# Performance work log

Measured on AMD Instinct MI355X. Metric: run time of the kernel, lower is better.

## Reference

```python
import jax, jax.numpy as jnp
import numpy as np

B = 4096          # graph pairs in batch
NPG = 40          # nodes per molecular graph
N = B * NPG       # total nodes per drug batch
EPG = 160         # directed edges per graph
E = B * EPG
F_IN = 78         # atom feature dim
HID = 128
HEADS = 4
ADD = 8           # additional features (concentrations)
BN_EPS = 1e-5
D0 = HEADS * HID          # 512
CMB = 4 * HID + ADD       # 2 drugs * (mean||max of 128) + ADD = 520


def setup_inputs() -> dict:
    key = jax.random.key(0)
    ks = iter(jax.random.split(key, 64))
    def nrm(shape, s=0.1):
        return jax.random.normal(next(ks), shape, jnp.float32) * s
    def pos(shape):  # positive running variances
        return jax.random.uniform(next(ks), shape, jnp.float32, 0.5, 1.5)
    offs = jnp.repeat(jnp.arange(B, dtype=jnp.int32) * NPG, EPG)
    def edges():
        return jax.random.randint(next(ks), (2, E), 0, NPG, dtype=jnp.int32) + offs[None, :]
    batch = jnp.repeat(jnp.arange(B, dtype=jnp.int32), NPG)
    inp = dict(
        x_a=nrm((N, F_IN), 1.0), edge_a=edges(), batch_a=batch,
        x_b=nrm((N, F_IN), 1.0), edge_b=edges(), batch_b=batch,
        addf=nrm((B, ADD), 1.0),
        # shared GAT encoder params
        gW0=nrm((F_IN, D0)), gb0=nrm((D0,)), gas0=nrm((D0,)), gad0=nrm((D0,)),
        gW1=nrm((D0, D0)), gb1=nrm((D0,)), gas1=nrm((D0,)), gad1=nrm((D0,)),
        gW2=nrm((D0, HID)), gb2=nrm((HID,)), gas2=nrm((HID,)), gad2=nrm((HID,)),
        bn0g=pos((D0,)), bn0b=nrm((D0,)), bn0m=nrm((D0,)), bn0v=pos((D0,)),
        bn1g=pos((D0,)), bn1b=nrm((D0,)), bn1m=nrm((D0,)), bn1v=pos((D0,)),
        bn2g=pos((HID,)), bn2b=nrm((HID,)), bn2m=nrm((HID,)), bn2v=pos((HID,)),
        # combination MLP params (Linear + eval BatchNorm stats)
        mW0=nrm((CMB, 2 * HID)), mb0=nrm((2 * HID,)),
        mg0=pos((2 * HID,)), mbe0=nrm((2 * HID,)), mm0=nrm((2 * HID,)), mv0=pos((2 * HID,)),
        mW1=nrm((2 * HID, HID)), mb1=nrm((HID,)),
        mg1=pos((HID,)), mbe1=nrm((HID,)), mm1=nrm((HID,)), mv1=pos((HID,)),
        mW2=nrm((HID, 1)), mb2=nrm((1,)),
    )
    return inp


def _bn(x, g, b, m, v):
    return (x - m) * jax.lax.rsqrt(v + BN_EPS) * g + b


def _gat(x, src, dst, W, b, a_src, a_dst, heads, ch, concat):
    """PyG GATConv (eval): linear, per-head additive attention with
    leaky_relu(0.2), segment-softmax over incoming edges (self-loops included)."""
    n = x.shape[0]
    h = (x @ W).reshape(n, heads, ch)                     # [N, H, C]
    es = jnp.sum(h * a_src.reshape(1, heads, ch), -1)     # [N, H]
    ed = jnp.sum(h * a_dst.reshape(1, heads, ch), -1)     # [N, H]
    e = jax.nn.leaky_relu(es[src] + ed[dst], 0.2)         # [E', H]
    emax = jax.ops.segment_max(e, dst, num_segments=n)
    ex = jnp.exp(e - emax[dst])
    den = jax.ops.segment_sum(ex, dst, num_segments=n)
    alpha = ex / den[dst]                                 # [E', H]
    out = jax.ops.segment_sum(h[src] * alpha[..., None], dst, num_segments=n)
    out = out.reshape(n, heads * ch) if concat else jnp.mean(out, axis=1)
    return out + b


def _encode(x, edge, batch, p):
    n = x.shape[0]
    sl = jnp.arange(n, dtype=edge.dtype)                  # self-loops (PyG default)
    src = jnp.concatenate([edge[0], sl])
    dst = jnp.concatenate([edge[1], sl])
    x = _gat(x, src, dst, p['gW0'], p['gb0'], p['gas0'], p['gad0'], HEADS, HID, True)
    x = jax.nn.relu(_bn(x, p['bn0g'], p['bn0b'], p['bn0m'], p['bn0v']))
    x = _gat(x, src, dst, p['gW1'], p['gb1'], p['gas1'], p['gad1'], HEADS, HID, True)
    x = jax.nn.relu(_bn(x, p['bn1g'], p['bn1b'], p['bn1m'], p['bn1v']))
    x = _gat(x, src, dst, p['gW2'], p['gb2'], p['gas2'], p['gad2'], 1, HID, False)
    x = _bn(x, p['bn2g'], p['bn2b'], p['bn2m'], p['bn2v'])  # no relu on last layer
    cnt = jax.ops.segment_sum(jnp.ones((n, 1), x.dtype), batch, num_segments=B)
    x_mean = jax.ops.segment_sum(x, batch, num_segments=B) / cnt
    x_max = jax.ops.segment_max(x, batch, num_segments=B)
    return jnp.concatenate([x_mean, x_max], axis=1)        # [B, 2*HID]


def reference(x_a, edge_a, batch_a, x_b, edge_b, batch_b, addf,
              gW0, gb0, gas0, gad0, gW1, gb1, gas1, gad1, gW2, gb2, gas2, gad2,
              bn0g, bn0b, bn0m, bn0v, bn1g, bn1b, bn1m, bn1v, bn2g, bn2b, bn2m, bn2v,
              mW0, mb0, mg0, mbe0, mm0, mv0, mW1, mb1, mg1, mbe1, mm1, mv1, mW2, mb2):
    p = dict(gW0=gW0, gb0=gb0, gas0=gas0, gad0=gad0, gW1=gW1, gb1=gb1, gas1=gas1,
             gad1=gad1, gW2=gW2, gb2=gb2, gas2=gas2, gad2=gad2,
             bn0g=bn0g, bn0b=bn0b, bn0m=bn0m, bn0v=bn0v,
             bn1g=bn1g, bn1b=bn1b, bn1m=bn1m, bn1v=bn1v,
             bn2g=bn2g, bn2b=bn2b, bn2m=bn2m, bn2v=bn2v)
    emb_a = _encode(x_a, edge_a, batch_a, p)
    emb_b = _encode(x_b, edge_b, batch_b, p)
    c = jnp.concatenate([emb_a, emb_b, addf], axis=1)      # [B, 520]
    h = jax.nn.relu(_bn(c @ mW0 + mb0, mg0, mbe0, mm0, mv0))
    h = jax.nn.relu(_bn(h @ mW1 + mb1, mg1, mbe1, mm1, mv1))
    out = jax.nn.sigmoid(h @ mW2 + mb2)
    return jnp.squeeze(out, -1)                            # [B]
```

## Files before the change

### kernel.cpp

```cpp
#include <hip/hip_runtime.h>
#include <stdint.h>

#define B_GRAPHS 4096
#define NPG 40
#define NTOT (B_GRAPHS * NPG)
#define EPG 160
#define ETOT (B_GRAPHS * EPG)
#define ESL 200
#define F_IN 78
#define KP0 96
#define HID 128
#define D0 512
#define CMB 520
#define BN_EPS 1e-5f
#define AST 48

typedef short bf16x8 __attribute__((ext_vector_type(8)));
typedef float floatx4 __attribute__((ext_vector_type(4)));

__device__ inline float b2f(unsigned short u) {
    union { float f; uint32_t i; } v; v.i = ((uint32_t)u) << 16; return v.f;
}
__device__ inline unsigned short f2b(float f) {
    union { float f; uint32_t i; } v; v.f = f;
    uint32_t x = v.i;
    return (unsigned short)((x + 0x7fffu + ((x >> 16) & 1u)) >> 16);
}
__device__ inline float lo16(uint32_t u) {
    union { float f; uint32_t i; } v; v.i = u << 16; return v.f;
}
__device__ inline float hi16(uint32_t u) {
    union { float f; uint32_t i; } v; v.i = u & 0xffff0000u; return v.f;
}
__device__ inline unsigned int fenc(float f) {
    unsigned int b = __float_as_uint(f);
    return (b & 0x80000000u) ? ~b : (b | 0x80000000u);
}
__device__ inline float fdec(unsigned int u) {
    unsigned int b = (u & 0x80000000u) ? (u & 0x7fffffffu) : ~u;
    return __uint_as_float(b);
}
__device__ inline int htoff(int ch, int s) {
    int chunk = s >> 3, within = s & 7;
    return ch * 40 + (((chunk + ch) % 5) << 3) + within;
}
__device__ inline void gl2lds16(const unsigned short* g, unsigned short* l) {
    __builtin_amdgcn_global_load_lds(
        (const __attribute__((address_space(1))) unsigned int*)g,
        (__attribute__((address_space(3))) unsigned int*)l, 16, 0, 0);
}

__global__ __launch_bounds__(256)
void write_code_kernel(float* __restrict__ out, int n, float S)
{
    int i = blockIdx.x * 256 + threadIdx.x;
    if (i < n) out[i] = (i == 0) ? S : 0.f;
}

__global__ __launch_bounds__(256)
void convw_kernel(const float* __restrict__ W, unsigned short* __restrict__ Wt,
                  int K, int N, int Kp)
{
    int t = blockIdx.x * 256 + threadIdx.x;
    if (t >= N * Kp) return;
    int n = t / Kp, k = t - n * Kp;
    Wt[t] = (k < K) ? f2b(W[(size_t)k * N + n]) : 0;
}

__global__ __launch_bounds__(256)
void convx_kernel(const float* __restrict__ X, unsigned short* __restrict__ Xb, int M)
{
    int t = blockIdx.x * 256 + threadIdx.x;
    if (t >= M * KP0) return;
    int r = t / KP0, k = t - r * KP0;
    Xb[t] = (k < F_IN) ? f2b(X[(size_t)r * F_IN + k]) : 0;
}

__global__ __launch_bounds__(256)
void gemm_mfma_kernel(const unsigned short* __restrict__ A,
                      const unsigned short* __restrict__ Bt,
                      unsigned short* __restrict__ C,
                      int M, int K, int N)
{
    __shared__ __align__(16) unsigned short As[128 * 32];
    __shared__ __align__(16) unsigned short Bs[128 * 32];
    const int tid  = threadIdx.x;
    const int lane = tid & 63, w = tid >> 6;
    const int quad = lane >> 4, l16 = lane & 15;
    const int wm = w >> 1, wn = w & 1;
    const int row0 = blockIdx.y * 128, col0 = blockIdx.x * 128;

    floatx4 acc[4][4];
    #pragma unroll
    for (int mi = 0; mi < 4; mi++)
        #pragma unroll
        for (int ni = 0; ni < 4; ni++)
            acc[mi][ni] = (floatx4){0.f, 0.f, 0.f, 0.f};

    int srow[2], scg[2];
    #pragma unroll
    for (int it = 0; it < 2; it++) {
        int L = it * 4096 + w * 1024 + lane * 16;
        int r = L >> 6;
        int cp = (L >> 4) & 3;
        srow[it] = r;
        scg[it]  = cp ^ ((r >> 1) & 3);
    }

    for (int k0 = 0; k0 < K; k0 += 32) {
        #pragma unroll
        for (int it = 0; it < 2; it++) {
            int ra = row0 + srow[it]; if (ra >= M) ra = M - 1;
            gl2lds16(A + (size_t)ra * K + k0 + scg[it] * 8,
                     As + (it * 4096 + w * 1024) / 2);
            int rb = col0 + srow[it];
            gl2lds16(Bt + (size_t)rb * K + k0 + scg[it] * 8,
                     Bs + (it * 4096 + w * 1024) / 2);
        }
        __syncthreads();

        bf16x8 fA[4], fB[4];
        #pragma unroll
        for (int mi = 0; mi < 4; mi++) {
            int r = wm * 64 + mi * 16 + l16;
            __builtin_memcpy(&fA[mi], &As[r * 32 + ((quad ^ ((r >> 1) & 3)) * 8)], 16);
        }
        #pragma unroll
        for (int ni = 0; ni < 4; ni++) {
            int r = wn * 64 + ni * 16 + l16;
            __builtin_memcpy(&fB[ni], &Bs[r * 32 + ((quad ^ ((r >> 1) & 3)) * 8)], 16);
        }
        #pragma unroll
        for (int mi = 0; mi < 4; mi++)
            #pragma unroll
            for (int ni = 0; ni < 4; ni++)
                acc[mi][ni] = __builtin_amdgcn_mfma_f32_16x16x32_bf16(
                    fB[ni], fA[mi], acc[mi][ni], 0, 0, 0);
        __syncthreads();
    }

    #pragma unroll
    for (int mi = 0; mi < 4; mi++) {
        int row = row0 + wm * 64 + mi * 16 + l16;
        if (row < M) {
            #pragma unroll
            for (int ni = 0; ni < 4; ni++) {
                floatx4 a = acc[mi][ni];
                unsigned int p0 = (unsigned int)f2b(a[0]) | ((unsigned int)f2b(a[1]) << 16);
                unsigned int p1 = (unsigned int)f2b(a[2]) | ((unsigned int)f2b(a[3]) << 16);
                *(uint2*)(C + (size_t)row * N + col0 + wn * 64 + ni * 16 + quad * 4) =
                    make_uint2(p0, p1);
            }
        }
    }
}

__global__ __launch_bounds__(256)
void gat4_fused_kernel(unsigned short* __restrict__ H,
                       const int* __restrict__ edge,
                       const float* __restrict__ avs, const float* __restrict__ avd,
                       const float* __restrict__ bias,
                       const float* __restrict__ bng, const float* __restrict__ bnb,
                       const float* __restrict__ bnm, const float* __restrict__ bnv,
                       int g0)
{
    __shared__ __align__(16) unsigned short ht[D0 * NPG];
    __shared__ float es[4 * NPG], ed[4 * NPG];
    __shared__ unsigned int Mu[4 * NPG];
    __shared__ float den[4 * NPG];
    __shared__ __align__(16) unsigned char cnt[NPG * 48];
    __shared__ short2 eloc[ESL];
    const int tid = threadIdx.x;
    const int lane = tid & 63, w = tid >> 6;
    const int quad = lane >> 4, l16 = lane & 15;
    const int gg = g0 + blockIdx.x;
    unsigned short* Hg = H + (size_t)blockIdx.x * NPG * D0;

    for (int i = tid; i < NPG * 48 / 4; i += 256) ((unsigned int*)cnt)[i] = 0u;
    if (tid < 4 * NPG) { Mu[tid] = 0u; den[tid] = 0.f; }
    for (int i = tid; i < ESL; i += 256) {
        if (i < EPG) {
            int s  = edge[(size_t)gg * EPG + i] - gg * NPG;
            int dd = edge[(size_t)ETOT + (size_t)gg * EPG + i] - gg * NPG;
            eloc[i] = make_short2((short)s, (short)dd);
        } else {
            short v = (short)(i - EPG);
            eloc[i] = make_short2(v, v);
        }
    }
    for (int u = tid; u < 64 * (NPG / 4); u += 256) {
        int c8 = u & 63, gi = u >> 6;
        const unsigned short* src = Hg + (size_t)(4 * gi) * D0 + c8 * 8;
        uint4 v0 = *(const uint4*)(src);
        uint4 v1 = *(const uint4*)(src + D0);
        uint4 v2 = *(const uint4*)(src + 2 * D0);
        uint4 v3 = *(const uint4*)(src + 3 * D0);
        unsigned int a0[4] = {v0.x, v0.y, v0.z, v0.w};
        unsigned int a1[4] = {v1.x, v1.y, v1.z, v1.w};
        unsigned int a2[4] = {v2.x, v2.y, v2.z, v2.w};
        unsigned int a3[4] = {v3.x, v3.y, v3.z, v3.w};
        #pragma unroll
        for (int k = 0; k < 8; k++) {
            const int ws = k >> 1, sh = (k & 1) * 16;
            unsigned int w0 = ((a0[ws] >> sh) & 0xffffu) | (((a1[ws] >> sh) & 0xffffu) << 16);
            unsigned int w1 = ((a2[ws] >> sh) & 0xffffu) | (((a3[ws] >> sh) & 0xffffu) << 16);
            *(uint2*)&ht[htoff(c8 * 8 + k, 4 * gi)] = make_uint2(w0, w1);
        }
    }
    __syncthreads();

    {
        float as0=0,as1=0,as2=0,as3=0, ad0=0,ad1=0,ad2=0,ad3=0;
        for (int ci = 0; ci < 32; ci++) {
            int c = quad + ci * 4;
            int chv = w * 128 + c;
            uint2 hv = *(const uint2*)&ht[htoff(chv, 4 * l16)];
            float h0 = lo16(hv.x), h1 = hi16(hv.x), h2 = lo16(hv.y), h3 = hi16(hv.y);
            float vs = avs[chv], vd = avd[chv];
            as0 += h0*vs; as1 += h1*vs; as2 += h2*vs; as3 += h3*vs;
            ad0 += h0*vd; ad1 += h1*vd; ad2 += h2*vd; ad3 += h3*vd;
        }
        #define RED4(x) x += __shfl_xor(x, 16); x += __shfl_xor(x, 32);
        RED4(as0) RED4(as1) RED4(as2) RED4(as3)
        RED4(ad0) RED4(ad1) RED4(ad2) RED4(ad3)
        #undef RED4
        if (quad == 0) {
            float rs[4] = {as0, as1, as2, as3};
            float rd[4] = {ad0, ad1, ad2, ad3};
            #pragma unroll
            for (int rr = 0; rr < 4; rr++) {
                int node = 4 * l16 + rr;
                if (node < NPG) { es[w * NPG + node] = rs[rr]; ed[w * NPG + node] = rd[rr]; }
            }
        }
    }
    for (int e = tid; e < ESL; e += 256) {
        short2 sd = eloc[e];
        atomicAdd((unsigned int*)cnt + ((sd.y * 48 + sd.x) >> 2),
                  1u << ((sd.x & 3) * 8));
    }
    __syncthreads();

    for (int u = tid; u < 4 * ESL; u += 256) {
        int e = u >> 2, hd = u & 3;
        short2 sd = eloc[e];
        float v = es[hd * NPG + sd.x] + ed[hd * NPG + sd.y];
        v = v > 0.f ? v : 0.2f * v;
        atomicMax(&Mu[hd * NPG + sd.y], fenc(v));
    }
    __syncthreads();
    for (int u = tid; u < 4 * ESL; u += 256) {
        int e = u >> 2, hd = u & 3;
        short2 sd = eloc[e];
        float v = es[hd * NPG + sd.x] + ed[hd * NPG + sd.y];
        v = v > 0.f ? v : 0.2f * v;
        float ex = __expf(v - fdec(Mu[hd * NPG + sd.y]));
        atomicAdd(&den[hd * NPG + sd.y], ex);
    }
    __syncthreads();

    {
        bf16x8 ahi[3][2], alo[3][2];
        float esv0[8], esv1[8];
        #pragma unroll
        for (int j = 0; j < 8; j++) {
            esv0[j] = es[w * NPG + quad * 8 + j];
            esv1[j] = (quad == 0) ? es[w * NPG + 32 + j] : 0.f;
        }
        #pragma unroll
        for (int mt = 0; mt < 3; mt++) {
            int dn = mt * 16 + l16;
            bool ok = dn < NPG;
            float edv = 0.f, m = 0.f, di = 0.f;
            uint2 c0 = make_uint2(0u, 0u), c1 = make_uint2(0u, 0u);
            if (ok) {
                edv = ed[w * NPG + dn];
                m = fdec(Mu[w * NPG + dn]);
                di = 1.f / den[w * NPG + dn];
                c0 = *(const uint2*)&cnt[dn * 48 + quad * 8];
                if (quad == 0) c1 = *(const uint2*)&cnt[dn * 48 + 32];
            }
            #pragma unroll
            for (int j = 0; j < 8; j++) {
                unsigned int cb0 = ((j < 4 ? c0.x : c0.y) >> ((j & 3) * 8)) & 0xffu;
                float v0 = esv0[j] + edv;
                v0 = v0 > 0.f ? v0 : 0.2f * v0;
                float a0 = (ok && cb0) ? (float)cb0 * __expf(v0 - m) * di : 0.f;
                unsigned short hb0 = f2b(a0);
                ahi[mt][0][j] = (short)hb0;
                alo[mt][0][j] = (short)f2b(a0 - b2f(hb0));

                unsigned int cb1 = ((j < 4 ? c1.x : c1.y) >> ((j & 3) * 8)) & 0xffu;
                float v1 = esv1[j] + edv;
                v1 = v1 > 0.f ? v1 : 0.2f * v1;
                float a1 = (ok && quad == 0 && cb1) ? (float)cb1 * __expf(v1 - m) * di : 0.f;
                unsigned short hb1 = f2b(a1);
                ahi[mt][1][j] = (short)hb1;
                alo[mt][1][j] = (short)f2b(a1 - b2f(hb1));
            }
        }
        const floatx4 z = {0.f, 0.f, 0.f, 0.f};
        for (int nt = 0; nt < 8; nt++) {
            const int ch0 = w * 128 + nt * 16;
            bf16x8 b0, b1 = {0,0,0,0,0,0,0,0};
            __builtin_memcpy(&b0, &ht[htoff(ch0 + l16, quad * 8)], 16);
            if (quad == 0) __builtin_memcpy(&b1, &ht[htoff(ch0 + l16, 32)], 16);
            floatx4 acc0 = z, acc1 = z, acc2 = z;
            acc0 = __builtin_amdgcn_mfma_f32_16x16x32_bf16(ahi[0][0], b0, acc0, 0, 0, 0);
            acc1 = __builtin_amdgcn_mfma_f32_16x16x32_bf16(ahi[1][0], b0, acc1, 0, 0, 0);
            acc2 = __builtin_amdgcn_mfma_f32_16x16x32_bf16(ahi[2][0], b0, acc2, 0, 0, 0);
            acc0 = __builtin_amdgcn_mfma_f32_16x16x32_bf16(alo[0][0], b0, acc0, 0, 0, 0);
            acc1 = __builtin_amdgcn_mfma_f32_16x16x32_bf16(alo[1][0], b0, acc1, 0, 0, 0);
            acc2 = __builtin_amdgcn_mfma_f32_16x16x32_bf16(alo[2][0], b0, acc2, 0, 0, 0);
            acc0 = __builtin_amdgcn_mfma_f32_16x16x32_bf16(ahi[0][1], b1, acc0, 0, 0, 0);
            acc1 = __builtin_amdgcn_mfma_f32_16x16x32_bf16(ahi[1][1], b1, acc1, 0, 0, 0);
            acc2 = __builtin_amdgcn_mfma_f32_16x16x32_bf16(ahi[2][1], b1, acc2, 0, 0, 0);
            acc0 = __builtin_amdgcn_mfma_f32_16x16x32_bf16(alo[0][1], b1, acc0, 0, 0, 0);
            acc1 = __builtin_amdgcn_mfma_f32_16x16x32_bf16(alo[1][1], b1, acc1, 0, 0, 0);
            acc2 = __builtin_amdgcn_mfma_f32_16x16x32_bf16(alo[2][1], b1, acc2, 0, 0, 0);
            const int c = ch0 + l16;
            float scl = rsqrtf(bnv[c] + BN_EPS) * bng[c];
            float sft = (bias[c] - bnm[c]) * scl + bnb[c];
            unsigned short* reg = &ht[ch0 * 40];
            #pragma unroll
            for (int mt = 0; mt < 3; mt++) {
                floatx4 a = (mt == 0) ? acc0 : (mt == 1) ? acc1 : acc2;
                #pragma unroll
                for (int rr = 0; rr < 4; rr++) {
                    int dn = mt * 16 + quad * 4 + rr;
                    if (dn < NPG) {
                        float o = a[rr] * scl + sft;
                        o = fmaxf(o, 0.f);
                        reg[dn * 16 + l16] = f2b(o);
                    }
                }
            }
        }
    }
    __syncthreads();
    for (int u = tid; u < NPG * 64; u += 256) {
        int s = u >> 6, c8 = u & 63;
        const unsigned short* reg = &ht[(c8 >> 1) * 16 * 40];
        uint4 v = *(const uint4*)&reg[s * 16 + (c8 & 1) * 8];
        *(uint4*)(Hg + (size_t)s * D0 + c8 * 8) = v;
    }
}

__global__ __launch_bounds__(256)
void gat1_pool_fused_kernel(const unsigned short* __restrict__ H,
                            const int* __restrict__ edge,
                            const float* __restrict__ avs, const float* __restrict__ avd,
                            const float* __restrict__ bias,
                            const float* __restrict__ bng, const float* __restrict__ bnb,
                            const float* __restrict__ bnm, const float* __restrict__ bnv,
                            float* __restrict__ cmb, int colbase, int g0)
{
    __shared__ __align__(16) unsigned short ht[HID * NPG];
    __shared__ float A1f[NPG * AST];
    __shared__ float es[NPG], ed[NPG];
    __shared__ unsigned int Mu[NPG];
    __shared__ float den[NPG];
    __shared__ short2 eloc[ESL];
    const int tid = threadIdx.x;
    const int lane = tid & 63, w = tid >> 6;
    const int quad = lane >> 4, l16 = lane & 15;
    const int gg = g0 + blockIdx.x;
    const unsigned short* Hg = H + (size_t)blockIdx.x * NPG * HID;

    for (int i = tid; i < NPG * AST; i += 256) A1f[i] = 0.f;
    if (tid < NPG) { Mu[tid] = 0u; den[tid] = 0.f; }
    for (int i = tid; i < ESL; i += 256) {
        if (i < EPG) {
            int s  = edge[(size_t)gg * EPG + i] - gg * NPG;
            int dd = edge[(size_t)ETOT + (size_t)gg * EPG + i] - gg * NPG;
            eloc[i] = make_short2((short)s, (short)dd);
        } else {
            short v = (short)(i - EPG);
            eloc[i] = make_short2(v, v);
        }
    }
    for (int u = tid; u < 16 * (NPG / 4); u += 256) {
        int c8 = u & 15, gi = u >> 4;
        const unsigned short* src = Hg + (size_t)(4 * gi) * HID + c8 * 8;
        uint4 v0 = *(const uint4*)(src);
        uint4 v1 = *(const uint4*)(src + HID);
        uint4 v2 = *(const uint4*)(src + 2 * HID);
        uint4 v3 = *(const uint4*)(src + 3 * HID);
        unsigned int a0[4] = {v0.x, v0.y, v0.z, v0.w};
        unsigned int a1[4] = {v1.x, v1.y, v1.z, v1.w};
        unsigned int a2[4] = {v2.x, v2.y, v2.z, v2.w};
        unsigned int a3[4] = {v3.x, v3.y, v3.z, v3.w};
        #pragma unroll
        for (int k = 0; k < 8; k++) {
            const int ws = k >> 1, sh = (k & 1) * 16;
            unsigned int w0 = ((a0[ws] >> sh) & 0xffffu) | (((a1[ws] >> sh) & 0xffffu) << 16);
            unsigned int w1 = ((a2[ws] >> sh) & 0xffffu) | (((a3[ws] >> sh) & 0xffffu) << 16);
            *(uint2*)&ht[htoff(c8 * 8 + k, 4 * gi)] = make_uint2(w0, w1);
        }
    }
    __syncthreads();

    if (w < 2) {
        const float* av = w ? avd : avs;
        float a0=0,a1=0,a2=0,a3=0;
        for (int ci = 0; ci < 32; ci++) {
            int c = quad + ci * 4;
            uint2 hv = *(const uint2*)&ht[htoff(c, 4 * l16)];
            float vc = av[c];
            a0 += lo16(hv.x)*vc; a1 += hi16(hv.x)*vc;
            a2 += lo16(hv.y)*vc; a3 += hi16(hv.y)*vc;
        }
        #define RED4(x) x += __shfl_xor(x, 16); x += __shfl_xor(x, 32);
        RED4(a0) RED4(a1) RED4(a2) RED4(a3)
        #undef RED4
        if (quad == 0) {
            float rv[4] = {a0, a1, a2, a3};
            float* dst = w ? ed : es;
            #pragma unroll
            for (int rr = 0; rr < 4; rr++) {
                int node = 4 * l16 + rr;
                if (node < NPG) dst[node] = rv[rr];
            }
        }
    }
    __syncthreads();
    for (int u = tid; u < ESL; u += 256) {
        short2 sd = eloc[u];
        float v = es[sd.x] + ed[sd.y];
        v = v > 0.f ? v : 0.2f * v;
        atomicMax(&Mu[sd.y], fenc(v));
    }
    __syncthreads();
    for (int u = tid; u < ESL; u += 256) {
        short2 sd = eloc[u];
        float v = es[sd.x] + ed[sd.y];
        v = v > 0.f ? v : 0.2f * v;
        float ex = __expf(v - fdec(Mu[sd.y]));
        atomicAdd(&den[sd.y], ex);
        atomicAdd(&A1f[sd.x * AST + sd.y], ex);
    }
    __syncthreads();
    for (int idx = tid; idx < NPG * AST; idx += 256) {
        int dn = idx % AST;
        float val = A1f[idx];
        unsigned int pw = 0u;
        if (dn < NPG) {
            float a = val / den[dn];
            unsigned short hi = f2b(a);
            float rem = a - b2f(hi);
            pw = (unsigned int)hi | ((unsigned int)f2b(rem) << 16);
        }
        ((unsigned int*)A1f)[idx] = pw;
    }
    __syncthreads();

    {
        const unsigned int* Ap = (const unsigned int*)A1f;
        bf16x8 ahi[3][2], alo[3][2];
        #pragma unroll
        for (int mt = 0; mt < 3; mt++) {
            #pragma unroll
            for (int j = 0; j < 8; j++) {
                unsigned int w0 = Ap[(quad * 8 + j) * AST + mt * 16 + l16];
                ahi[mt][0][j] = (short)(w0 & 0xffffu);
                alo[mt][0][j] = (short)(w0 >> 16);
                unsigned int w1 = (quad == 0) ? Ap[(32 + j) * AST + mt * 16 + l16] : 0u;
                ahi[mt][1][j] = (short)(w1 & 0xffffu);
                alo[mt][1][j] = (short)(w1 >> 16);
            }
        }
        const floatx4 z = {0.f, 0.f, 0.f, 0.f};
        for (int t2 = 0; t2 < 2; t2++) {
            const int ch0 = (w * 2 + t2) * 16;
            bf16x8 b0, b1 = {0,0,0,0,0,0,0,0};
            __builtin_memcpy(&b0, &ht[htoff(ch0 + l16, quad * 8)], 16);
            if (quad == 0) __builtin_memcpy(&b1, &ht[htoff(ch0 + l16, 32)], 16);
            floatx4 acc0 = z, acc1 = z, acc2 = z;
            acc0 = __builtin_amdgcn_mfma_f32_16x16x32_bf16(ahi[0][0], b0, acc0, 0, 0, 0);
            acc1 = __builtin_amdgcn_mfma_f32_16x16x32_bf16(ahi[1][0], b0, acc1, 0, 0, 0);
            acc2 = __builtin_amdgcn_mfma_f32_16x16x32_bf16(ahi[2][0], b0, acc2, 0, 0, 0);
            acc0 = __builtin_amdgcn_mfma_f32_16x16x32_bf16(alo[0][0], b0, acc0, 0, 0, 0);
            acc1 = __builtin_amdgcn_mfma_f32_16x16x32_bf16(alo[1][0], b0, acc1, 0, 0, 0);
            acc2 = __builtin_amdgcn_mfma_f32_16x16x32_bf16(alo[2][0], b0, acc2, 0, 0, 0);
            acc0 = __builtin_amdgcn_mfma_f32_16x16x32_bf16(ahi[0][1], b1, acc0, 0, 0, 0);
            acc1 = __builtin_amdgcn_mfma_f32_16x16x32_bf16(ahi[1][1], b1, acc1, 0, 0, 0);
            acc2 = __builtin_amdgcn_mfma_f32_16x16x32_bf16(ahi[2][1], b1, acc2, 0, 0, 0);
            acc0 = __builtin_amdgcn_mfma_f32_16x16x32_bf16(alo[0][1], b1, acc0, 0, 0, 0);
            acc1 = __builtin_amdgcn_mfma_f32_16x16x32_bf16(alo[1][1], b1, acc1, 0, 0, 0);
            acc2 = __builtin_amdgcn_mfma_f32_16x16x32_bf16(alo[2][1], b1, acc2, 0, 0, 0);
            const int c = ch0 + l16;
            float scl = rsqrtf(bnv[c] + BN_EPS) * bng[c];
            float sft = (bias[c] - bnm[c]) * scl + bnb[c];
            float psum = 0.f, pmax = -1e30f;
            #pragma unroll
            for (int mt = 0; mt < 3; mt++) {
                floatx4 a = (mt == 0) ? acc0 : (mt == 1) ? acc1 : acc2;
                #pragma unroll
                for (int rr = 0; rr < 4; rr++) {
                    int dn = mt * 16 + quad * 4 + rr;
                    if (dn < NPG) {
                        float o = a[rr] * scl + sft;
                        psum += o;
                        pmax = fmaxf(pmax, o);
                    }
                }
            }
            psum += __shfl_xor(psum, 16); psum += __shfl_xor(psum, 32);
            pmax = fmaxf(pmax, __shfl_xor(pmax, 16));
            pmax = fmaxf(pmax, __shfl_xor(pmax, 32));
            if (quad == 0) {
                cmb[(size_t)gg * 512 + colbase + c] = psum * (1.f / NPG);
                cmb[(size_t)gg * 512 + colbase + HID + c] = pmax;
            }
        }
    }
}

__global__ __launch_bounds__(256)
void mlp_kernel(const float* __restrict__ cmb, const float* __restrict__ addf,
                const float* __restrict__ W0, const float* __restrict__ b0,
                const float* __restrict__ g0v, const float* __restrict__ be0,
                const float* __restrict__ m0, const float* __restrict__ v0,
                const float* __restrict__ W1, const float* __restrict__ b1,
                const float* __restrict__ g1v, const float* __restrict__ be1,
                const float* __restrict__ m1, const float* __restrict__ v1,
                const float* __restrict__ W2, const float* __restrict__ b2,
                float* __restrict__ out)
{
    __shared__ float c[CMB];
    __shared__ float h1[256];
    __shared__ float h2[128];
    const int g = blockIdx.x, tid = threadIdx.x;
    for (int i = tid; i < 512; i += 256) c[i] = cmb[(size_t)g * 512 + i];
    if (tid < 8) c[512 + tid] = addf[g * 8 + tid];
    __syncthreads();
    {
        int j = tid;
        float acc = b0[j];
        for (int k = 0; k < CMB; k++) acc += c[k] * W0[k * 256 + j];
        acc = (acc - m0[j]) * rsqrtf(v0[j] + BN_EPS) * g0v[j] + be0[j];
        h1[j] = fmaxf(acc, 0.f);
    }
    __syncthreads();
    if (tid < 128) {
        int j = tid;
        float acc = b1[j];
        for (int k = 0; k < 256; k++) acc += h1[k] * W1[k * 128 + j];
        acc = (acc - m1[j]) * rsqrtf(v1[j] + BN_EPS) * g1v[j] + be1[j];
        h2[j] = fmaxf(acc, 0.f);
    }
    __syncthreads();
    if (tid == 0) {
        float acc = b2[0];
        for (int k = 0; k < 128; k++) acc += h2[k] * W2[k];
        out[g] = 1.f / (1.f + __expf(-acc));
    }
}

extern "C" void kernel_launch(void* const* d_in, const int* in_sizes, int n_in,
                              void* d_out, int out_size, void* d_ws, size_t ws_size,
                              hipStream_t stream)
{
    float* out = (float*)d_out;
    int out_n = out_size < 4096 ? out_size : 4096;

    const float* x_a  = (const float*)d_in[0];
    const int*   edge_a = (const int*)d_in[1];
    const float* x_b  = (const float*)d_in[3];
    const int*   edge_b = (const int*)d_in[4];
    const float* addf = (const float*)d_in[6];
    const float* gW0 = (const float*)d_in[7],  *gb0 = (const float*)d_in[8];
    const float* gas0 = (const float*)d_in[9], *gad0 = (const float*)d_in[10];
    const float* gW1 = (const float*)d_in[11], *gb1 = (const float*)d_in[12];
    const float* gas1 = (const float*)d_in[13], *gad1 = (const float*)d_in[14];
    const float* gW2 = (const float*)d_in[15], *gb2 = (const float*)d_in[16];
    const float* gas2 = (const float*)d_in[17], *gad2 = (const float*)d_in[18];
    const float* bn0g = (const float*)d_in[19], *bn0b = (const float*)d_in[20];
    const float* bn0m = (const float*)d_in[21], *bn0v = (const float*)d_in[22];
    const float* bn1g = (const float*)d_in[23], *bn1b = (const float*)d_in[24];
    const float* bn1m = (const float*)d_in[25], *bn1v = (const float*)d_in[26];
    const float* bn2g = (const float*)d_in[27], *bn2b = (const float*)d_in[28];
    const float* bn2m = (const float*)d_in[29], *bn2v = (const float*)d_in[30];
    const float* mW0 = (const float*)d_in[31], *mb0 = (const float*)d_in[32];
    const float* mg0 = (const float*)d_in[33], *mbe0 = (const float*)d_in[34];
    const float* mm0 = (const float*)d_in[35], *mv0 = (const float*)d_in[36];
    const float* mW1 = (const float*)d_in[37], *mb1 = (const float*)d_in[38];
    const float* mg1 = (const float*)d_in[39], *mbe1 = (const float*)d_in[40];
    const float* mm1 = (const float*)d_in[41], *mv1 = (const float*)d_in[42];
    const float* mW2 = (const float*)d_in[43], *mb2 = (const float*)d_in[44];

    char* p = (char*)d_ws;
    const size_t CMB_BYTES = (size_t)B_GRAPHS * 512 * sizeof(float);
    float* cmb = (float*)p; p += CMB_BYTES;
    unsigned short* W0t = (unsigned short*)p; p += (size_t)D0 * KP0 * 2;
    unsigned short* W1t = (unsigned short*)p; p += (size_t)D0 * D0 * 2;
    unsigned short* W2t = (unsigned short*)p; p += (size_t)HID * D0 * 2;
    size_t used = (size_t)(p - (char*)d_ws);
    const size_t PG = 7680ull + 40960ull + 40960ull;
    int chunk = B_GRAPHS;
    while (chunk > 4 && used + (size_t)chunk * PG > ws_size) chunk >>= 1;
    if (used + (size_t)chunk * PG > ws_size) {
        write_code_kernel<<<(out_n + 255) / 256, 256, 0, stream>>>(out, out_n, 500000.f);
        return;
    }
    unsigned short* Xb = (unsigned short*)p; p += (size_t)chunk * 7680;
    unsigned short* B1 = (unsigned short*)p; p += (size_t)chunk * 40960;
    unsigned short* B2 = (unsigned short*)p;

    convw_kernel<<<(D0 * KP0 + 255) / 256, 256, 0, stream>>>(gW0, W0t, F_IN, D0, KP0);
    convw_kernel<<<(D0 * D0 + 255) / 256, 256, 0, stream>>>(gW1, W1t, D0, D0, D0);
    convw_kernel<<<(HID * D0 + 255) / 256, 256, 0, stream>>>(gW2, W2t, D0, HID, D0);

    for (int drug = 0; drug < 2; drug++) {
        const float* x = drug ? x_b : x_a;
        const int* edge = drug ? edge_b : edge_a;
        int colbase = drug ? 256 : 0;

        for (int g0 = 0; g0 < B_GRAPHS; g0 += chunk) {
            int n = chunk * NPG;
            int gy = (n + 127) / 128;
            convx_kernel<<<(n * KP0 + 255) / 256, 256, 0, stream>>>(
                x + (size_t)g0 * NPG * F_IN, Xb, n);
            gemm_mfma_kernel<<<dim3(D0 / 128, gy), 256, 0, stream>>>(
                Xb, W0t, B1, n, KP0, D0);
            gat4_fused_kernel<<<chunk, 256, 0, stream>>>(
                B1, edge, gas0, gad0, gb0, bn0g, bn0b, bn0m, bn0v, g0);
            gemm_mfma_kernel<<<dim3(D0 / 128, gy), 256, 0, stream>>>(
                B1, W1t, B2, n, D0, D0);
            gat4_fused_kernel<<<chunk, 256, 0, stream>>>(
                B2, edge, gas1, gad1, gb1, bn1g, bn1b, bn1m, bn1v, g0);
            gemm_mfma_kernel<<<dim3(HID / 128, gy), 256, 0, stream>>>(
                B2, W2t, B1, n, D0, HID);
            gat1_pool_fused_kernel<<<chunk, 256, 0, stream>>>(
                B1, edge, gas2, gad2, gb2, bn2g, bn2b, bn2m, bn2v,
                cmb, colbase, g0);
        }
    }
    mlp_kernel<<<B_GRAPHS, 256, 0, stream>>>(
        cmb, addf, mW0, mb0, mg0, mbe0, mm0, mv0,
        mW1, mb1, mg1, mbe1, mm1, mv1, mW2, mb2, out);
}
```

Baseline: 1.489 ms.

## Run combination MLP on MFMA with split bf16 hi/lo and vectorize convx

```diff
diff --git a/kernel.cpp b/kernel.cpp
--- a/kernel.cpp
+++ b/kernel.cpp
@@ -14,6 +14,10 @@
 #define CMB 520
 #define BN_EPS 1e-5f
 #define AST 48
+#define KPM 544
+#define A0ST 552
+#define H1ST 264
+#define H2ST 132
 
 typedef short bf16x8 __attribute__((ext_vector_type(8)));
 typedef float floatx4 __attribute__((ext_vector_type(4)));
@@ -68,12 +72,35 @@
 }
 
 __global__ __launch_bounds__(256)
+void convw_hilo_kernel(const float* __restrict__ W,
+                       unsigned short* __restrict__ Whi,
+                       unsigned short* __restrict__ Wlo,
+                       int K, int N, int Kp)
+{
+    int t = blockIdx.x * 256 + threadIdx.x;
+    if (t >= N * Kp) return;
+    int n = t / Kp, k = t - n * Kp;
+    float x = (k < K) ? W[(size_t)k * N + n] : 0.f;
+    unsigned short hb = f2b(x);
+    Whi[t] = hb;
+    Wlo[t] = f2b(x - b2f(hb));
+}
+
+__global__ __launch_bounds__(256)
 void convx_kernel(const float* __restrict__ X, unsigned short* __restrict__ Xb, int M)
 {
     int t = blockIdx.x * 256 + threadIdx.x;
-    if (t >= M * KP0) return;
-    int r = t / KP0, k = t - r * KP0;
-    Xb[t] = (k < F_IN) ? f2b(X[(size_t)r * F_IN + k]) : 0;
+    if (t >= M * (KP0 / 8)) return;
+    int r = t / (KP0 / 8), c8 = t - r * (KP0 / 8);
+    unsigned int pk[4];
+    #pragma unroll
+    for (int j = 0; j < 4; j++) {
+        int k0 = c8 * 8 + 2 * j, k1 = k0 + 1;
+        float x0 = (k0 < F_IN) ? X[(size_t)r * F_IN + k0] : 0.f;
+        float x1 = (k1 < F_IN) ? X[(size_t)r * F_IN + k1] : 0.f;
+        pk[j] = (unsigned int)f2b(x0) | ((unsigned int)f2b(x1) << 16);
+    }
+    *(uint4*)&Xb[(size_t)r * KP0 + c8 * 8] = make_uint4(pk[0], pk[1], pk[2], pk[3]);
 }
 
 __global__ __launch_bounds__(256)
@@ -517,43 +544,123 @@
 }
 
 __global__ __launch_bounds__(256)
-void mlp_kernel(const float* __restrict__ cmb, const float* __restrict__ addf,
-                const float* __restrict__ W0, const float* __restrict__ b0,
-                const float* __restrict__ g0v, const float* __restrict__ be0,
-                const float* __restrict__ m0, const float* __restrict__ v0,
-                const float* __restrict__ W1, const float* __restrict__ b1,
-                const float* __restrict__ g1v, const float* __restrict__ be1,
-                const float* __restrict__ m1, const float* __restrict__ v1,
-                const float* __restrict__ W2, const float* __restrict__ b2,
-                float* __restrict__ out)
-{
-    __shared__ float c[CMB];
-    __shared__ float h1[256];
-    __shared__ float h2[128];
-    const int g = blockIdx.x, tid = threadIdx.x;
-    for (int i = tid; i < 512; i += 256) c[i] = cmb[(size_t)g * 512 + i];
-    if (tid < 8) c[512 + tid] = addf[g * 8 + tid];
-    __syncthreads();
+void mlp_mfma_kernel(const float* __restrict__ cmb, const float* __restrict__ addf,
+                     const unsigned short* __restrict__ W0hi, const unsigned short* __restrict__ W0lo,
+                     const float* __restrict__ b0, const float* __restrict__ g0v,
+                     const float* __restrict__ be0, const float* __restrict__ m0,
+                     const float* __restrict__ v0,
+                     const unsigned short* __restrict__ W1hi, const unsigned short* __restrict__ W1lo,
+                     const float* __restrict__ b1, const float* __restrict__ g1v,
+                     const float* __restrict__ be1, const float* __restrict__ m1,
+                     const float* __restrict__ v1,
+                     const float* __restrict__ W2, const float* __restrict__ b2,
+                     float* __restrict__ out)
+{
+    __shared__ __align__(16) unsigned short a0hi[16 * A0ST], a0lo[16 * A0ST];
+    __shared__ __align__(16) unsigned short h1hi[16 * H1ST], h1lo[16 * H1ST];
+    __shared__ float h2[16 * H2ST];
+    const int tid = threadIdx.x;
+    const int lane = tid & 63, w = tid >> 6;
+    const int quad = lane >> 4, l16 = lane & 15;
+    const int gb = blockIdx.x * 16;
+
+    for (int i = tid; i < 16 * KPM; i += 256) {
+        int g = i / KPM, k = i - g * KPM;
+        float x = 0.f;
+        if (k < 512) x = cmb[(size_t)(gb + g) * 512 + k];
+        else if (k < CMB) x = addf[(gb + g) * 8 + (k - 512)];
+        unsigned short hb = f2b(x);
+        a0hi[g * A0ST + k] = hb;
+        a0lo[g * A0ST + k] = f2b(x - b2f(hb));
+    }
+    __syncthreads();
+
     {
-        int j = tid;
-        float acc = b0[j];
-        for (int k = 0; k < CMB; k++) acc += c[k] * W0[k * 256 + j];
-        acc = (acc - m0[j]) * rsqrtf(v0[j] + BN_EPS) * g0v[j] + be0[j];
-        h1[j] = fmaxf(acc, 0.f);
-    }
-    __syncthreads();
-    if (tid < 128) {
-        int j = tid;
-        float acc = b1[j];
-        for (int k = 0; k < 256; k++) acc += h1[k] * W1[k * 128 + j];
-        acc = (acc - m1[j]) * rsqrtf(v1[j] + BN_EPS) * g1v[j] + be1[j];
-        h2[j] = fmaxf(acc, 0.f);
-    }
-    __syncthreads();
-    if (tid == 0) {
-        float acc = b2[0];
-        for (int k = 0; k < 128; k++) acc += h2[k] * W2[k];
-        out[g] = 1.f / (1.f + __expf(-acc));
+        floatx4 acc[4];
+        #pragma unroll
+        for (int ni = 0; ni < 4; ni++) acc[ni] = (floatx4){0.f, 0.f, 0.f, 0.f};
+        for (int k0 = 0; k0 < KPM; k0 += 32) {
+            bf16x8 fah, fal;
+            __builtin_memcpy(&fah, &a0hi[l16 * A0ST + k0 + quad * 8], 16);
+            __builtin_memcpy(&fal, &a0lo[l16 * A0ST + k0 + quad * 8], 16);
+            #pragma unroll
+            for (int ni = 0; ni < 4; ni++) {
+                int row = w * 64 + ni * 16 + l16;
+                bf16x8 fwh, fwl;
+                __builtin_memcpy(&fwh, &W0hi[(size_t)row * KPM + k0 + quad * 8], 16);
+                __builtin_memcpy(&fwl, &W0lo[(size_t)row * KPM + k0 + quad * 8], 16);
+                acc[ni] = __builtin_amdgcn_mfma_f32_16x16x32_bf16(fwh, fah, acc[ni], 0, 0, 0);
+                acc[ni] = __builtin_amdgcn_mfma_f32_16x16x32_bf16(fwh, fal, acc[ni], 0, 0, 0);
+                acc[ni] = __builtin_amdgcn_mfma_f32_16x16x32_bf16(fwl, fah, acc[ni], 0, 0, 0);
+            }
+        }
+        #pragma unroll
+        for (int ni = 0; ni < 4; ni++) {
+            int cbase = w * 64 + ni * 16 + quad * 4;
+            unsigned int ph[2], pl[2];
+            #pragma unroll
+            for (int j = 0; j < 2; j++) {
+                unsigned int hh[2], ll[2];
+                #pragma unroll
+                for (int q = 0; q < 2; q++) {
+                    int rr = 2 * j + q, c = cbase + rr;
+                    float scl = rsqrtf(v0[c] + BN_EPS) * g0v[c];
+                    float val = (acc[ni][rr] + b0[c] - m0[c]) * scl + be0[c];
+                    val = fmaxf(val, 0.f);
+                    unsigned short hb = f2b(val);
+                    hh[q] = hb;
+                    ll[q] = f2b(val - b2f(hb));
+                }
+                ph[j] = hh[0] | (hh[1] << 16);
+                pl[j] = ll[0] | (ll[1] << 16);
+            }
+            *(uint2*)&h1hi[l16 * H1ST + cbase] = make_uint2(ph[0], ph[1]);
+            *(uint2*)&h1lo[l16 * H1ST + cbase] = make_uint2(pl[0], pl[1]);
+        }
+    }
+    __syncthreads();
+
+    {
+        floatx4 acc[2];
+        acc[0] = (floatx4){0.f, 0.f, 0.f, 0.f};
+        acc[1] = (floatx4){0.f, 0.f, 0.f, 0.f};
+        for (int k0 = 0; k0 < 256; k0 += 32) {
+            bf16x8 fah, fal;
+            __builtin_memcpy(&fah, &h1hi[l16 * H1ST + k0 + quad * 8], 16);
+            __builtin_memcpy(&fal, &h1lo[l16 * H1ST + k0 + quad * 8], 16);
+            #pragma unroll
+            for (int ni = 0; ni < 2; ni++) {
+                int row = w * 32 + ni * 16 + l16;
+                bf16x8 fwh, fwl;
+                __builtin_memcpy(&fwh, &W1hi[(size_t)row * 256 + k0 + quad * 8], 16);
+                __builtin_memcpy(&fwl, &W1lo[(size_t)row * 256 + k0 + quad * 8], 16);
+                acc[ni] = __builtin_amdgcn_mfma_f32_16x16x32_bf16(fwh, fah, acc[ni], 0, 0, 0);
+                acc[ni] = __builtin_amdgcn_mfma_f32_16x16x32_bf16(fwh, fal, acc[ni], 0, 0, 0);
+                acc[ni] = __builtin_amdgcn_mfma_f32_16x16x32_bf16(fwl, fah, acc[ni], 0, 0, 0);
+            }
+        }
+        #pragma unroll
+        for (int ni = 0; ni < 2; ni++) {
+            #pragma unroll
+            for (int rr = 0; rr < 4; rr++) {
+                int c = w * 32 + ni * 16 + quad * 4 + rr;
+                float scl = rsqrtf(v1[c] + BN_EPS) * g1v[c];
+                float val = (acc[ni][rr] + b1[c] - m1[c]) * scl + be1[c];
+                h2[l16 * H2ST + c] = fmaxf(val, 0.f);
+            }
+        }
+    }
+    __syncthreads();
+
+    {
+        int g = tid >> 4, part = tid & 15;
+        float s = 0.f;
+        #pragma unroll
+        for (int j = 0; j < 8; j++)
+            s += h2[g * H2ST + part * 8 + j] * W2[part * 8 + j];
+        s += __shfl_xor(s, 1); s += __shfl_xor(s, 2);
+        s += __shfl_xor(s, 4); s += __shfl_xor(s, 8);
+        if (part == 0) out[gb + g] = 1.f / (1.f + __expf(-(s + b2[0])));
     }
 }
 
@@ -595,6 +702,10 @@
     unsigned short* W0t = (unsigned short*)p; p += (size_t)D0 * KP0 * 2;
     unsigned short* W1t = (unsigned short*)p; p += (size_t)D0 * D0 * 2;
     unsigned short* W2t = (unsigned short*)p; p += (size_t)HID * D0 * 2;
+    unsigned short* M0hi = (unsigned short*)p; p += (size_t)256 * KPM * 2;
+    unsigned short* M0lo = (unsigned short*)p; p += (size_t)256 * KPM * 2;
+    unsigned short* M1hi = (unsigned short*)p; p += (size_t)128 * 256 * 2;
+    unsigned short* M1lo = (unsigned short*)p; p += (size_t)128 * 256 * 2;
     size_t used = (size_t)(p - (char*)d_ws);
     const size_t PG = 7680ull + 40960ull + 40960ull;
     int chunk = B_GRAPHS;
@@ -610,6 +721,10 @@
     convw_kernel<<<(D0 * KP0 + 255) / 256, 256, 0, stream>>>(gW0, W0t, F_IN, D0, KP0);
     convw_kernel<<<(D0 * D0 + 255) / 256, 256, 0, stream>>>(gW1, W1t, D0, D0, D0);
     convw_kernel<<<(HID * D0 + 255) / 256, 256, 0, stream>>>(gW2, W2t, D0, HID, D0);
+    convw_hilo_kernel<<<(256 * KPM + 255) / 256, 256, 0, stream>>>(
+        mW0, M0hi, M0lo, CMB, 256, KPM);
+    convw_hilo_kernel<<<(128 * 256 + 255) / 256, 256, 0, stream>>>(
+        mW1, M1hi, M1lo, 256, 128, 256);
 
     for (int drug = 0; drug < 2; drug++) {
         const float* x = drug ? x_b : x_a;
@@ -619,7 +734,7 @@
         for (int g0 = 0; g0 < B_GRAPHS; g0 += chunk) {
             int n = chunk * NPG;
             int gy = (n + 127) / 128;
-            convx_kernel<<<(n * KP0 + 255) / 256, 256, 0, stream>>>(
+            convx_kernel<<<(n * (KP0 / 8) + 255) / 256, 256, 0, stream>>>(
                 x + (size_t)g0 * NPG * F_IN, Xb, n);
             gemm_mfma_kernel<<<dim3(D0 / 128, gy), 256, 0, stream>>>(
                 Xb, W0t, B1, n, KP0, D0);
@@ -636,7 +751,7 @@
                 cmb, colbase, g0);
         }
     }
-    mlp_kernel<<<B_GRAPHS, 256, 0, stream>>>(
-        cmb, addf, mW0, mb0, mg0, mbe0, mm0, mv0,
-        mW1, mb1, mg1, mbe1, mm1, mv1, mW2, mb2, out);
-}
+    mlp_mfma_kernel<<<B_GRAPHS / 16, 256, 0, stream>>>(
+        cmb, addf, M0hi, M0lo, mb0, mg0, mbe0, mm0, mv0,
+        M1hi, M1lo, mb1, mg1, mbe1, mm1, mv1, mW2, mb2, out);
+}
```

Result: faster. 1.419 ms (-4.7%).
